# Optimization experiments

Hardware: AMD Instinct MI355X
Metric: run time of the kernel (lower is better)

## Reference

```python
import jax, jax.numpy as jnp
import numpy as np

B, L, V, D, H, DK, NL, M = 4, 1024, 64, 256, 4, 64, 4, 20
FF = 4 * D
EPS = 1e-5


def _rel_table(seq_len, m):
    # abs(i-j), log-bucketed beyond m, clipped to [0, 2m] -> int indices [L, L]
    d = jnp.abs(jnp.arange(seq_len)[:, None] - jnp.arange(seq_len)[None, :]).astype(jnp.float32)
    d = jnp.where(d > m, m + jnp.log2(jnp.maximum(d - m, 1.0)), d)
    return jnp.clip(d, 0, 2 * m).astype(jnp.int32)


def _layer_norm(x, g, b):
    mu = jnp.mean(x, axis=-1, keepdims=True)
    var = jnp.mean(jnp.square(x - mu), axis=-1, keepdims=True)
    return (x - mu) * jax.lax.rsqrt(var + EPS) * g + b


def setup_inputs() -> dict:
    key = jax.random.key(0)
    ks = jax.random.split(key, 16)
    w = lambda i, shape: jax.random.normal(ks[i], shape, jnp.float32) * 0.05
    return {
        "x": jax.random.normal(ks[0], (B, L, V), jnp.float32),
        "emb": w(1, (V, D)),
        "Wq": w(2, (NL, D, H * DK)), "bq": jnp.zeros((NL, H * DK), jnp.float32),
        "Wk": w(3, (NL, D, H * DK)), "bk": jnp.zeros((NL, H * DK), jnp.float32),
        "Wv": w(4, (NL, D, H * DK)), "bv": jnp.zeros((NL, H * DK), jnp.float32),
        "Wo": w(5, (NL, H * DK, D)), "bo": jnp.zeros((NL, D), jnp.float32),
        "rel_k": 1.0 + w(6, (NL, 2 * M + 1, H)),  # multiplicative bias ~1
        "rel_b": w(7, (NL, 2 * M + 1, H)),
        "ln1_g": jnp.ones((NL, D), jnp.float32), "ln1_b": jnp.zeros((NL, D), jnp.float32),
        "W1": w(8, (NL, D, FF)), "b1": jnp.zeros((NL, FF), jnp.float32),
        "W2": w(9, (NL, FF, D)), "b2": jnp.zeros((NL, D), jnp.float32),
        "ln2_g": jnp.ones((NL, D), jnp.float32), "ln2_b": jnp.zeros((NL, D), jnp.float32),
    }


def reference(x, emb, Wq, bq, Wk, bk, Wv, bv, Wo, bo, rel_k, rel_b,
              ln1_g, ln1_b, W1, b1, W2, b2, ln2_g, ln2_b):
    h = x @ emb  # [B, L, D]  (dropout inactive: eval mode)
    table = _rel_table(L, M)  # [L, L] int32
    inv_sqrt_dk = jnp.float32(1.0 / np.sqrt(DK))
    attns = []
    for l in range(NL):
        q = (h @ Wq[l] + bq[l]).reshape(B, L, H, DK)
        k = (h @ Wk[l] + bk[l]).reshape(B, L, H, DK)
        v = (h @ Wv[l] + bv[l]).reshape(B, L, H, DK)
        scores = jnp.einsum('blhk,bmhk->bhlm', q, k) * inv_sqrt_dk
        # per-head relative-position bias (table symmetric, so axis order of L,L is immaterial)
        bias_k = jnp.transpose(rel_k[l][table], (2, 1, 0))  # [H, L, L]
        bias_b = jnp.transpose(rel_b[l][table], (2, 1, 0))  # [H, L, L]
        scores = scores * bias_k[None] + bias_b[None]
        attn = jax.nn.softmax(scores, axis=-1)  # attn dropout inactive (eval)
        attns.append(attn)
        out = jnp.einsum('bhlm,bmhk->blhk', attn, v).reshape(B, L, H * DK) @ Wo[l] + bo[l]
        # FeedForwardNetwork (note: source has NO residual connections)
        y = _layer_norm(out, ln1_g[l], ln1_b[l])
        y = jax.nn.gelu(y @ W1[l] + b1[l], approximate=False) @ W2[l] + b2[l]
        h = _layer_norm(y, ln2_g[l], ln2_b[l])
    avg_attn = jnp.mean(jnp.stack(attns, axis=0), axis=0)  # [B, H, L, L]
    return h.mean(axis=1), avg_attn
```

## Files before the change

kernel.cpp:

```cpp
#include <hip/hip_runtime.h>
#include <hip/hip_bf16.h>
#include <math.h>

#define Bn 4
#define Ln 1024
#define Vn 64
#define Dn 256
#define Hn 4
#define DKn 64
#define NLn 4
#define Mn 20
#define FFn 1024
#define NTOK (Bn * Ln)
#define QKVW 768
#define LOG2E 1.4426950408889634f
#define PELEMS (Bn * Hn * Ln * Ln)

typedef __attribute__((ext_vector_type(8))) short bf16x8;
typedef __attribute__((ext_vector_type(4))) float f32x4;

__device__ __forceinline__ ushort f2b(float f) {
    uint u = __float_as_uint(f);
    u += 0x7fff + ((u >> 16) & 1);
    return (ushort)(u >> 16);
}
__device__ __forceinline__ float b2f(ushort u) {
    return __uint_as_float(((uint)u) << 16);
}

__global__ __launch_bounds__(256) void embed_k(const float* __restrict__ X,
                                               const float* __restrict__ E,
                                               ushort* __restrict__ Hb) {
    __shared__ float xs[Vn];
    int n = blockIdx.x, d = threadIdx.x;
    if (threadIdx.x < Vn) xs[threadIdx.x] = X[n * Vn + threadIdx.x];
    __syncthreads();
    float s = 0.f;
#pragma unroll
    for (int v = 0; v < Vn; ++v) s += xs[v] * E[v * Dn + d];
    Hb[(size_t)n * Dn + d] = f2b(s);
}

__global__ __launch_bounds__(256) void relbias_k(const float* __restrict__ rk,
                                                 const float* __restrict__ rb,
                                                 float* __restrict__ bkT,
                                                 float* __restrict__ bbT) {
    int tid = blockIdx.x * 256 + threadIdx.x;
    int dist = tid & 1023;
    int hh = (tid >> 10) & 3;
    int l = tid >> 12;
    float dd = (float)dist;
    if (dist > Mn) dd = (float)Mn + log2f((float)(dist - Mn));
    if (dd > 2.0f * Mn) dd = 2.0f * Mn;
    int idx = (int)dd;
    bkT[tid] = rk[(l * (2 * Mn + 1) + idx) * Hn + hh] * 0.125f * LOG2E;
    bbT[tid] = rb[(l * (2 * Mn + 1) + idx) * Hn + hh] * LOG2E;
}

__global__ __launch_bounds__(256) void prep_bias(const float* __restrict__ bq,
                                                 const float* __restrict__ bk,
                                                 const float* __restrict__ bv,
                                                 float* __restrict__ bqkv) {
    int idx = blockIdx.x * 256 + threadIdx.x;
    int l = idx / QKVW, r = idx - l * QKVW;
    float v;
    if (r < 256)      v = bq[l * 256 + r];
    else if (r < 512) v = bk[l * 256 + r - 256];
    else              v = bv[l * 256 + r - 512];
    bqkv[idx] = v;
}

__global__ __launch_bounds__(256) void transpose_cvt(
    const float* __restrict__ src, ushort* __restrict__ dst,
    int R, int C, int srcLS, int dstLS) {
    __shared__ float s[32][33];
    src += (size_t)blockIdx.z * srcLS;
    dst += (size_t)blockIdx.z * dstLS;
    int r0 = blockIdx.y * 32, c0 = blockIdx.x * 32;
    int tx = threadIdx.x & 31, ty = threadIdx.x >> 5;
#pragma unroll
    for (int ii = 0; ii < 4; ++ii)
        s[ty + 8 * ii][tx] = src[(size_t)(r0 + ty + 8 * ii) * C + c0 + tx];
    __syncthreads();
#pragma unroll
    for (int ii = 0; ii < 4; ++ii)
        dst[(size_t)(c0 + ty + 8 * ii) * R + r0 + tx] = f2b(s[tx][ty + 8 * ii]);
}

__global__ __launch_bounds__(256) void transpose_v(const ushort* __restrict__ qkv,
                                                   ushort* __restrict__ Vt) {
    __shared__ ushort s[32][65];
    int j0 = blockIdx.x * 32;
    int bh = blockIdx.y;
    int b = bh >> 2, hh = bh & 3;
    int t = threadIdx.x;
#pragma unroll
    for (int ii = 0; ii < 8; ++ii) {
        int e = t + 256 * ii;
        int jr = e >> 6, dc = e & 63;
        s[jr][dc] = qkv[(size_t)(b * Ln + j0 + jr) * QKVW + 2 * Dn + hh * DKn + dc];
    }
    __syncthreads();
#pragma unroll
    for (int ii = 0; ii < 8; ++ii) {
        int e = t + 256 * ii;
        int dr = e >> 5, jc = e & 31;
        Vt[(size_t)(bh * DKn + dr) * Ln + j0 + jc] = s[jc][dr];
    }
}

#define GST 40
#define GEMM_FRAG_MFMA                                                        \
    bf16x8 a0 = *(const bf16x8*)&As[(wm * 32 + l15) * GST + lg * 8];          \
    bf16x8 a1 = *(const bf16x8*)&As[(wm * 32 + 16 + l15) * GST + lg * 8];     \
    bf16x8 b0 = *(const bf16x8*)&Bs[(wn * 32 + l15) * GST + lg * 8];          \
    bf16x8 b1 = *(const bf16x8*)&Bs[(wn * 32 + 16 + l15) * GST + lg * 8];     \
    acc[0][0] = __builtin_amdgcn_mfma_f32_16x16x32_bf16(a0, b0, acc[0][0], 0, 0, 0); \
    acc[0][1] = __builtin_amdgcn_mfma_f32_16x16x32_bf16(a0, b1, acc[0][1], 0, 0, 0); \
    acc[1][0] = __builtin_amdgcn_mfma_f32_16x16x32_bf16(a1, b0, acc[1][0], 0, 0, 0); \
    acc[1][1] = __builtin_amdgcn_mfma_f32_16x16x32_bf16(a1, b1, acc[1][1], 0, 0, 0);

template <int LNA>
__global__ __launch_bounds__(256) void gemm_mfma(
    const ushort* __restrict__ A, const ushort* __restrict__ Bt,
    const float* __restrict__ bias, ushort* __restrict__ C,
    int M, int N, int K, int act,
    const float* __restrict__ lng, const float* __restrict__ lnb) {
    __shared__ __align__(16) ushort As[64 * GST];
    __shared__ __align__(16) ushort Bs[64 * GST];
    __shared__ float gl[256];
    __shared__ float bl[256];
    int t = threadIdx.x;
    int lane = t & 63, w = t >> 6;
    int wm = w >> 1, wn = w & 1;
    int l15 = lane & 15, lg = lane >> 4;
    int mBase = blockIdx.y * 64, nBase = blockIdx.x * 64;
    int lrow = t >> 2, lkc = (t & 3) * 8;
    const ushort* Ap = A + (size_t)(mBase + lrow) * K + lkc;
    const ushort* Bp = Bt + (size_t)(nBase + lrow) * K + lkc;
    f32x4 acc[2][2] = {};

    if constexpr (LNA) {
        uint4 areg[8];
        float s = 0.f;
#pragma unroll
        for (int kc = 0; kc < 8; ++kc) {
            areg[kc] = *(const uint4*)(Ap + kc * 32);
            const ushort* e = (const ushort*)&areg[kc];
#pragma unroll
            for (int q = 0; q < 8; ++q) s += b2f(e[q]);
        }
        s += __shfl_xor(s, 1, 64);
        s += __shfl_xor(s, 2, 64);
        float mu = s * (1.0f / 256.0f);
        float vv = 0.f;
#pragma unroll
        for (int kc = 0; kc < 8; ++kc) {
            const ushort* e = (const ushort*)&areg[kc];
#pragma unroll
            for (int q = 0; q < 8; ++q) {
                float d = b2f(e[q]) - mu;
                vv += d * d;
            }
        }
        vv += __shfl_xor(vv, 1, 64);
        vv += __shfl_xor(vv, 2, 64);
        float rs = rsqrtf(vv * (1.0f / 256.0f) + 1e-5f);
        gl[t] = lng[t];
        bl[t] = lnb[t];
        __syncthreads();
#pragma unroll
        for (int kc = 0; kc < 8; ++kc) {
            uint4 bv = *(const uint4*)(Bp + kc * 32);
            __syncthreads();
            {
                const ushort* e = (const ushort*)&areg[kc];
                ushort outv[8];
#pragma unroll
                for (int q = 0; q < 8; ++q) {
                    int col = kc * 32 + lkc + q;
                    outv[q] = f2b((b2f(e[q]) - mu) * rs * gl[col] + bl[col]);
                }
                *(uint4*)&As[lrow * GST + lkc] = *(const uint4*)outv;
            }
            *(uint4*)&Bs[lrow * GST + lkc] = bv;
            __syncthreads();
            GEMM_FRAG_MFMA
        }
    } else {
        for (int k0 = 0; k0 < K; k0 += 32) {
            uint4 av = *(const uint4*)(Ap + k0);
            uint4 bv = *(const uint4*)(Bp + k0);
            __syncthreads();
            *(uint4*)&As[lrow * GST + lkc] = av;
            *(uint4*)&Bs[lrow * GST + lkc] = bv;
            __syncthreads();
            GEMM_FRAG_MFMA
        }
    }
#pragma unroll
    for (int ni = 0; ni < 2; ++ni) {
        int col = nBase + wn * 32 + ni * 16 + l15;
        float bc = bias[col];
#pragma unroll
        for (int mi = 0; mi < 2; ++mi) {
            int rb = mBase + wm * 32 + mi * 16 + lg * 4;
#pragma unroll
            for (int j = 0; j < 4; ++j) {
                float v = acc[mi][ni][j] + bc;
                if (act) v = v * 0.5f * (1.0f + erff(v * 0.7071067811865475f));
                C[(size_t)(rb + j) * N + col] = f2b(v);
            }
        }
    }
}

#define PWST 40
#define NW 8
template <int MODE>
__global__ __launch_bounds__(512) void attn_fused(
    const ushort* __restrict__ qkv, const ushort* __restrict__ Vt,
    const float* __restrict__ bkTab, const float* __restrict__ bbTab,
    ushort* __restrict__ ctx, float* __restrict__ avg,
    ushort* __restrict__ Pout, int first) {
    __shared__ float bk_l[Ln];
    __shared__ float bb_l[Ln];
    __shared__ __align__(16) char uni[NW][4096];
    __shared__ float mm[NW][16];
    __shared__ float ll[NW][16];

    int t = threadIdx.x;
    int lane = t & 63, w = t >> 6;
    int wn = w & 3, wc = w >> 2;
    int l15 = lane & 15, lg = lane >> 4;

    ushort* pwh = (ushort*)&uni[w][0];
    ushort* pwl = (ushort*)&uni[w][1280];

    int bid = blockIdx.x;
    int xcd = bid & 7, sub = bid >> 3;
    int bh = xcd * 2 + (sub >> 6);
    int q = sub & 63;
    int b = bh >> 2, hh = bh & 3;
    int i0 = q * 16;

#pragma unroll
    for (int ii = 0; ii < 2; ++ii) {
        bk_l[t + 512 * ii] = bkTab[hh * Ln + t + 512 * ii];
        bb_l[t + 512 * ii] = bbTab[hh * Ln + t + 512 * ii];
    }
    __syncthreads();

    bf16x8 qa0, qa1;
    {
        const ushort* qp = qkv + (size_t)(b * Ln + i0 + l15) * QKVW + hh * DKn;
        qa0 = *(const bf16x8*)(qp + lg * 8);
        qa1 = *(const bf16x8*)(qp + 32 + lg * 8);
    }

    const ushort* kbase = qkv + (size_t)(b * Ln) * QKVW + Dn + hh * DKn;

    f32x4 sv[8];
    float m[4] = {-1e30f, -1e30f, -1e30f, -1e30f};
#pragma unroll
    for (int cl = 0; cl < 8; ++cl) {
        int c = wc * 8 + cl;
        const ushort* kp = kbase + (size_t)(c * 64 + wn * 16 + l15) * QKVW;
        bf16x8 k0 = *(const bf16x8*)(kp + lg * 8);
        bf16x8 k1 = *(const bf16x8*)(kp + 32 + lg * 8);
        f32x4 acc = {};
        acc = __builtin_amdgcn_mfma_f32_16x16x32_bf16(qa0, k0, acc, 0, 0, 0);
        acc = __builtin_amdgcn_mfma_f32_16x16x32_bf16(qa1, k1, acc, 0, 0, 0);
        int j = c * 64 + wn * 16 + l15;
#pragma unroll
        for (int r = 0; r < 4; ++r) {
            int i = i0 + lg * 4 + r;
            int dist = (i > j) ? (i - j) : (j - i);
            float s = acc[r] * bk_l[dist] + bb_l[dist];
            sv[cl][r] = s;
            m[r] = fmaxf(m[r], s);
        }
    }
#pragma unroll
    for (int mask = 1; mask < 16; mask <<= 1)
#pragma unroll
        for (int r = 0; r < 4; ++r) m[r] = fmaxf(m[r], __shfl_xor(m[r], mask, 64));
    if (l15 == 0)
#pragma unroll
        for (int r = 0; r < 4; ++r) mm[w][lg * 4 + r] = m[r];
    __syncthreads();
#pragma unroll
    for (int r = 0; r < 4; ++r) {
        int row = lg * 4 + r;
        float m0 = fmaxf(fmaxf(mm[0][row], mm[1][row]), fmaxf(mm[2][row], mm[3][row]));
        float m1 = fmaxf(fmaxf(mm[4][row], mm[5][row]), fmaxf(mm[6][row], mm[7][row]));
        m[r] = fmaxf(m0, m1);
    }
    float lsum[4] = {0.f, 0.f, 0.f, 0.f};
#pragma unroll
    for (int cl = 0; cl < 8; ++cl)
#pragma unroll
        for (int r = 0; r < 4; ++r) {
            float p = exp2f(sv[cl][r] - m[r]);
            sv[cl][r] = p;
            lsum[r] += p;
        }
#pragma unroll
    for (int mask = 1; mask < 16; mask <<= 1)
#pragma unroll
        for (int r = 0; r < 4; ++r) lsum[r] += __shfl_xor(lsum[r], mask, 64);
    if (l15 == 0)
#pragma unroll
        for (int r = 0; r < 4; ++r) ll[w][lg * 4 + r] = lsum[r];
    __syncthreads();
    float invl[4];
#pragma unroll
    for (int r = 0; r < 4; ++r) {
        int row = lg * 4 + r;
        invl[r] = 1.0f / (ll[0][row] + ll[1][row] + ll[2][row] + ll[3][row] +
                          ll[4][row] + ll[5][row] + ll[6][row] + ll[7][row]);
    }

    const ushort* vbase = Vt + (size_t)bh * DKn * Ln;
    float* avgrow = avg + ((size_t)bh * Ln + i0) * Ln;
    ushort* prow = Pout + ((size_t)bh * Ln + i0) * Ln;
    int iw = lane >> 2, jq = lane & 3;
    f32x4 acco[4] = {};
#pragma unroll
    for (int p = 0; p < 4; ++p) {
        const int c0 = wc * 8 + 2 * p, c1 = c0 + 1;
        float aold[2][4];
        if (MODE == 0 && !first) {
#pragma unroll
            for (int cc = 0; cc < 2; ++cc)
#pragma unroll
                for (int r = 0; r < 4; ++r)
                    aold[cc][r] = avgrow[(size_t)(lg * 4 + r) * Ln +
                                         (c0 + cc) * 64 + wn * 16 + l15];
        }
#pragma unroll
        for (int cc = 0; cc < 2; ++cc)
#pragma unroll
            for (int r = 0; r < 4; ++r) {
                float pv = sv[2 * p + cc][r] * invl[r];
                sv[2 * p + cc][r] = pv;
                ushort ph = f2b(pv);
                int off = (lg * 4 + r) * PWST + cc * 16 + l15;
                pwh[off] = ph;
                pwl[off] = f2b(pv - b2f(ph));
            }
        int kcol = (lg < 2 ? c0 : c1) * 64 + wn * 16 + (lg & 1) * 8;
        bf16x8 va0 = *(const bf16x8*)(vbase + (size_t)(0 * 16 + l15) * Ln + kcol);
        bf16x8 va1 = *(const bf16x8*)(vbase + (size_t)(1 * 16 + l15) * Ln + kcol);
        bf16x8 va2 = *(const bf16x8*)(vbase + (size_t)(2 * 16 + l15) * Ln + kcol);
        bf16x8 va3 = *(const bf16x8*)(vbase + (size_t)(3 * 16 + l15) * Ln + kcol);
        bf16x8 pbh = *(const bf16x8*)&pwh[l15 * PWST + lg * 8];
        bf16x8 pbl = *(const bf16x8*)&pwl[l15 * PWST + lg * 8];
        acco[0] = __builtin_amdgcn_mfma_f32_16x16x32_bf16(va0, pbh, acco[0], 0, 0, 0);
        acco[1] = __builtin_amdgcn_mfma_f32_16x16x32_bf16(va1, pbh, acco[1], 0, 0, 0);
        acco[2] = __builtin_amdgcn_mfma_f32_16x16x32_bf16(va2, pbh, acco[2], 0, 0, 0);
        acco[3] = __builtin_amdgcn_mfma_f32_16x16x32_bf16(va3, pbh, acco[3], 0, 0, 0);
        acco[0] = __builtin_amdgcn_mfma_f32_16x16x32_bf16(va0, pbl, acco[0], 0, 0, 0);
        acco[1] = __builtin_amdgcn_mfma_f32_16x16x32_bf16(va1, pbl, acco[1], 0, 0, 0);
        acco[2] = __builtin_amdgcn_mfma_f32_16x16x32_bf16(va2, pbl, acco[2], 0, 0, 0);
        acco[3] = __builtin_amdgcn_mfma_f32_16x16x32_bf16(va3, pbl, acco[3], 0, 0, 0);
        if (MODE == 0) {
#pragma unroll
            for (int cc = 0; cc < 2; ++cc)
#pragma unroll
                for (int r = 0; r < 4; ++r) {
                    float v = 0.25f * sv[2 * p + cc][r];
                    if (!first) v += aold[cc][r];
                    avgrow[(size_t)(lg * 4 + r) * Ln + (c0 + cc) * 64 + wn * 16 + l15] = v;
                }
        } else {
            ushort4 ph0 = *(const ushort4*)&pwh[iw * PWST + 0 * 16 + jq * 4];
            ushort4 ph1 = *(const ushort4*)&pwh[iw * PWST + 1 * 16 + jq * 4];
            *(ushort4*)&prow[(size_t)iw * Ln + c0 * 64 + wn * 16 + jq * 4] = ph0;
            *(ushort4*)&prow[(size_t)iw * Ln + c1 * 64 + wn * 16 + jq * 4] = ph1;
        }
    }

    {
        float* op = (float*)&uni[w][0];
#pragma unroll
        for (int dg = 0; dg < 4; ++dg)
#pragma unroll
            for (int r = 0; r < 4; ++r)
                op[(dg * 16 + lg * 4 + r) * 16 + l15] = acco[dg][r];
    }
    __syncthreads();
#pragma unroll
    for (int k = 0; k < 2; ++k) {
        int idx = t + 512 * k;
        float v = 0.f;
#pragma unroll
        for (int wv = 0; wv < NW; ++wv) v += ((const float*)&uni[wv][0])[idx];
        int dd = idx >> 4, ii = idx & 15;
        ctx[(size_t)(b * Ln + i0 + ii) * Dn + hh * DKn + dd] = f2b(v);
    }
}

__global__ __launch_bounds__(256) void avg_sum_k(const ushort* __restrict__ P,
                                                 float* __restrict__ avg) {
    size_t e = ((size_t)blockIdx.x * 256 + threadIdx.x) * 8;
    uint4 a = *(const uint4*)&P[e];
    uint4 b4 = *(const uint4*)&P[(size_t)PELEMS + e];
    uint4 c4 = *(const uint4*)&P[(size_t)2 * PELEMS + e];
    uint4 d4 = *(const uint4*)&P[(size_t)3 * PELEMS + e];
    const ushort* ap = (const ushort*)&a;
    const ushort* bp = (const ushort*)&b4;
    const ushort* cp = (const ushort*)&c4;
    const ushort* dp = (const ushort*)&d4;
    float4 o0, o1;
    float* o0p = (float*)&o0;
    float* o1p = (float*)&o1;
#pragma unroll
    for (int k = 0; k < 4; ++k)
        o0p[k] = 0.25f * (b2f(ap[k]) + b2f(bp[k]) + b2f(cp[k]) + b2f(dp[k]));
#pragma unroll
    for (int k = 0; k < 4; ++k)
        o1p[k] = 0.25f * (b2f(ap[4 + k]) + b2f(bp[4 + k]) + b2f(cp[4 + k]) + b2f(dp[4 + k]));
    *(float4*)&avg[e] = o0;
    *(float4*)&avg[e + 4] = o1;
}

__global__ __launch_bounds__(256) void layernorm_k(const ushort* __restrict__ X,
                                                   const float* __restrict__ g,
                                                   const float* __restrict__ bta,
                                                   ushort* __restrict__ Y) {
    int w = threadIdx.x >> 6, lane = threadIdx.x & 63;
    int row = blockIdx.x * 4 + w;
    const ushort* xr = X + (size_t)row * Dn;
    float x[4];
#pragma unroll
    for (int ii = 0; ii < 4; ++ii) x[ii] = b2f(xr[lane + 64 * ii]);
    float s = x[0] + x[1] + x[2] + x[3];
#pragma unroll
    for (int m = 1; m < 64; m <<= 1) s += __shfl_xor(s, m, 64);
    float mu = s * (1.0f / 256.0f);
    float vs = 0.f;
#pragma unroll
    for (int ii = 0; ii < 4; ++ii) {
        float d = x[ii] - mu;
        vs += d * d;
    }
#pragma unroll
    for (int m = 1; m < 64; m <<= 1) vs += __shfl_xor(vs, m, 64);
    float rs = rsqrtf(vs * (1.0f / 256.0f) + 1e-5f);
#pragma unroll
    for (int ii = 0; ii < 4; ++ii) {
        int d = lane + 64 * ii;
        Y[(size_t)row * Dn + d] = f2b((x[ii] - mu) * rs * g[d] + bta[d]);
    }
}

__global__ __launch_bounds__(256) void mean_part_k(const ushort* __restrict__ Hb,
                                                   float* __restrict__ part) {
    int blk = blockIdx.x;
    int b = blk >> 4, g = blk & 15;
    int d = threadIdx.x;
    float s = 0.f;
#pragma unroll
    for (int r = 0; r < 64; ++r)
        s += b2f(Hb[(size_t)(b * Ln + g * 64 + r) * Dn + d]);
    part[(size_t)blk * Dn + d] = s;
}
__global__ __launch_bounds__(256) void mean_final_k(const float* __restrict__ part,
                                                    float* __restrict__ out) {
    int b = blockIdx.x, d = threadIdx.x;
    float s = 0.f;
#pragma unroll
    for (int g = 0; g < 16; ++g) s += part[(size_t)(b * 16 + g) * Dn + d];
    out[b * Dn + d] = s * (1.0f / (float)Ln);
}

extern "C" void kernel_launch(void* const* d_in, const int* in_sizes, int n_in,
                              void* d_out, int out_size, void* d_ws, size_t ws_size,
                              hipStream_t stream) {
    const float* x    = (const float*)d_in[0];
    const float* emb  = (const float*)d_in[1];
    const float* Wq   = (const float*)d_in[2];
    const float* bq   = (const float*)d_in[3];
    const float* Wk   = (const float*)d_in[4];
    const float* bk   = (const float*)d_in[5];
    const float* Wv   = (const float*)d_in[6];
    const float* bv   = (const float*)d_in[7];
    const float* Wo   = (const float*)d_in[8];
    const float* bo   = (const float*)d_in[9];
    const float* rk   = (const float*)d_in[10];
    const float* rb   = (const float*)d_in[11];
    const float* ln1g = (const float*)d_in[12];
    const float* ln1b = (const float*)d_in[13];
    const float* W1   = (const float*)d_in[14];
    const float* b1   = (const float*)d_in[15];
    const float* W2   = (const float*)d_in[16];
    const float* b2   = (const float*)d_in[17];
    const float* ln2g = (const float*)d_in[18];
    const float* ln2b = (const float*)d_in[19];

    float* out = (float*)d_out;
    float* avg = out + Bn * Dn;

    char* ws = (char*)d_ws;
    const size_t MB = 1024 * 1024;
    ushort* hb   = (ushort*)(ws);
    ushort* qkvb = (ushort*)(ws + 2 * MB);
    ushort* ctxb = (ushort*)(ws + 8 * MB);
    ushort* t1   = (ushort*)(ws + 10 * MB);
    ushort* ffb  = (ushort*)(ws + 12 * MB);
    ushort* qkvT = (ushort*)(ws + 20 * MB);
    ushort* WoT  = (ushort*)(ws + 22 * MB);
    ushort* W1T  = (ushort*)(ws + 23 * MB);
    ushort* W2T  = (ushort*)(ws + 25 * MB);
    float*  bqkv = (float*)(ws + 27 * MB);
    float*  bkT  = (float*)(ws + 27 * MB + 65536);
    float*  bbT  = (float*)(ws + 27 * MB + 131072);
    ushort* Vt   = (ushort*)(ws + 30 * MB);
    float*  mpart= (float*)(ws + 33 * MB);
    ushort* Pbuf = (ushort*)(ws + 36 * MB);

    const size_t need = 36 * MB + (size_t)4 * PELEMS * sizeof(ushort);
    const bool fancy = (ws_size >= need);

    embed_k<<<NTOK, 256, 0, stream>>>(x, emb, hb);
    relbias_k<<<64, 256, 0, stream>>>(rk, rb, bkT, bbT);
    prep_bias<<<12, 256, 0, stream>>>(bq, bk, bv, bqkv);

    dim3 t88(8, 8, NLn);
    transpose_cvt<<<t88, 256, 0, stream>>>(Wq, qkvT + 0,      256, 256, 65536, 196608);
    transpose_cvt<<<t88, 256, 0, stream>>>(Wk, qkvT + 65536,  256, 256, 65536, 196608);
    transpose_cvt<<<t88, 256, 0, stream>>>(Wv, qkvT + 131072, 256, 256, 65536, 196608);
    transpose_cvt<<<t88, 256, 0, stream>>>(Wo, WoT,           256, 256, 65536, 65536);
    transpose_cvt<<<dim3(32, 8, NLn), 256, 0, stream>>>(W1, W1T, 256, 1024, 262144, 262144);
    transpose_cvt<<<dim3(8, 32, NLn), 256, 0, stream>>>(W2, W2T, 1024, 256, 262144, 262144);

    for (int l = 0; l < NLn; ++l) {
        if (l == 0) {
            gemm_mfma<0><<<dim3(12, 64), 256, 0, stream>>>(
                hb, qkvT + (size_t)l * 196608, bqkv + l * QKVW, qkvb,
                NTOK, QKVW, Dn, 0, nullptr, nullptr);
        } else {
            gemm_mfma<1><<<dim3(12, 64), 256, 0, stream>>>(
                hb, qkvT + (size_t)l * 196608, bqkv + l * QKVW, qkvb,
                NTOK, QKVW, Dn, 0, ln2g + (l - 1) * 256, ln2b + (l - 1) * 256);
        }
        transpose_v<<<dim3(32, 16), 256, 0, stream>>>(qkvb, Vt);
        if (fancy) {
            attn_fused<1><<<1024, 512, 0, stream>>>(
                qkvb, Vt, bkT + l * Hn * Ln, bbT + l * Hn * Ln, ctxb, avg,
                Pbuf + (size_t)l * PELEMS, (l == 0) ? 1 : 0);
        } else {
            attn_fused<0><<<1024, 512, 0, stream>>>(
                qkvb, Vt, bkT + l * Hn * Ln, bbT + l * Hn * Ln, ctxb, avg,
                (ushort*)Pbuf, (l == 0) ? 1 : 0);
        }
        gemm_mfma<0><<<dim3(4, 64), 256, 0, stream>>>(
            ctxb, WoT + (size_t)l * 65536, bo + l * 256, t1,
            NTOK, Dn, Dn, 0, nullptr, nullptr);
        gemm_mfma<1><<<dim3(16, 64), 256, 0, stream>>>(
            t1, W1T + (size_t)l * 262144, b1 + l * FFn, ffb,
            NTOK, FFn, Dn, 1, ln1g + l * 256, ln1b + l * 256);
        gemm_mfma<0><<<dim3(4, 64), 256, 0, stream>>>(
            ffb, W2T + (size_t)l * 262144, b2 + l * 256, hb,
            NTOK, Dn, FFn, 0, nullptr, nullptr);
    }
    layernorm_k<<<NTOK / 4, 256, 0, stream>>>(
        hb, ln2g + 3 * 256, ln2b + 3 * 256, hb);
    if (fancy) {
        avg_sum_k<<<PELEMS / (256 * 8), 256, 0, stream>>>(Pbuf, avg);
    }
    mean_part_k<<<64, 256, 0, stream>>>(hb, mpart);
    mean_final_k<<<Bn, 256, 0, stream>>>(mpart, out);
}
```

Measured before the change: 416.1 us.

## Fuse V transpose into QKV GEMM and attention-average into last layer

The QKV GEMM epilogue now writes V directly in transposed layout for the V column blocks, so the separate transpose_v kernel is gone. The last layer's attention kernel reads the three stored bf16 probability maps, adds its own, and writes the fp32 average itself. This removes the avg_sum_k pass and the fourth P buffer. The attention context reduction across warps now goes through two-stage shared-memory accumulation into four slots instead of eight, which adds extra barriers. The QKV GEMM skips its normal C store for V columns, which is fine only as long as attention reads V solely from Vt.

```diff
diff --git a/kernel.cpp b/kernel.cpp
--- a/kernel.cpp
+++ b/kernel.cpp
@@ -87,28 +87,6 @@
         dst[(size_t)(c0 + ty + 8 * ii) * R + r0 + tx] = f2b(s[tx][ty + 8 * ii]);
 }
 
-__global__ __launch_bounds__(256) void transpose_v(const ushort* __restrict__ qkv,
-                                                   ushort* __restrict__ Vt) {
-    __shared__ ushort s[32][65];
-    int j0 = blockIdx.x * 32;
-    int bh = blockIdx.y;
-    int b = bh >> 2, hh = bh & 3;
-    int t = threadIdx.x;
-#pragma unroll
-    for (int ii = 0; ii < 8; ++ii) {
-        int e = t + 256 * ii;
-        int jr = e >> 6, dc = e & 63;
-        s[jr][dc] = qkv[(size_t)(b * Ln + j0 + jr) * QKVW + 2 * Dn + hh * DKn + dc];
-    }
-    __syncthreads();
-#pragma unroll
-    for (int ii = 0; ii < 8; ++ii) {
-        int e = t + 256 * ii;
-        int dr = e >> 5, jc = e & 31;
-        Vt[(size_t)(bh * DKn + dr) * Ln + j0 + jc] = s[jc][dr];
-    }
-}
-
 #define GST 40
 #define GEMM_FRAG_MFMA                                                        \
     bf16x8 a0 = *(const bf16x8*)&As[(wm * 32 + l15) * GST + lg * 8];          \
@@ -125,7 +103,8 @@
     const ushort* __restrict__ A, const ushort* __restrict__ Bt,
     const float* __restrict__ bias, ushort* __restrict__ C,
     int M, int N, int K, int act,
-    const float* __restrict__ lng, const float* __restrict__ lnb) {
+    const float* __restrict__ lng, const float* __restrict__ lnb,
+    ushort* __restrict__ Vt_out) {
     __shared__ __align__(16) ushort As[64 * GST];
     __shared__ __align__(16) ushort Bs[64 * GST];
     __shared__ float gl[256];
@@ -198,6 +177,25 @@
             GEMM_FRAG_MFMA
         }
     }
+    if (Vt_out != nullptr && nBase >= 512) {
+#pragma unroll
+        for (int ni = 0; ni < 2; ++ni) {
+            int col = nBase + wn * 32 + ni * 16 + l15;
+            float bc = bias[col];
+            int d = col - 512;
+#pragma unroll
+            for (int mi = 0; mi < 2; ++mi) {
+                int rb = mBase + wm * 32 + mi * 16 + lg * 4;
+                int bb_ = rb >> 10, i_ = rb & 1023;
+                size_t vb = ((size_t)(bb_ * 4 + (d >> 6)) * 64 + (d & 63)) * Ln + i_;
+                ushort o4[4];
+#pragma unroll
+                for (int j = 0; j < 4; ++j) o4[j] = f2b(acc[mi][ni][j] + bc);
+                *(ushort4*)&Vt_out[vb] = *(const ushort4*)o4;
+            }
+        }
+        return;
+    }
 #pragma unroll
     for (int ni = 0; ni < 2; ++ni) {
         int col = nBase + wn * 32 + ni * 16 + l15;
@@ -225,7 +223,7 @@
     ushort* __restrict__ Pout, int first) {
     __shared__ float bk_l[Ln];
     __shared__ float bb_l[Ln];
-    __shared__ __align__(16) char uni[NW][4096];
+    __shared__ __align__(16) char uni[20480];
     __shared__ float mm[NW][16];
     __shared__ float ll[NW][16];
 
@@ -234,8 +232,8 @@
     int wn = w & 3, wc = w >> 2;
     int l15 = lane & 15, lg = lane >> 4;
 
-    ushort* pwh = (ushort*)&uni[w][0];
-    ushort* pwl = (ushort*)&uni[w][1280];
+    ushort* pwh = (ushort*)&uni[w * 2560];
+    ushort* pwl = (ushort*)&uni[w * 2560 + 1280];
 
     int bid = blockIdx.x;
     int xcd = bid & 7, sub = bid >> 3;
@@ -373,56 +371,66 @@
                     if (!first) v += aold[cc][r];
                     avgrow[(size_t)(lg * 4 + r) * Ln + (c0 + cc) * 64 + wn * 16 + l15] = v;
                 }
-        } else {
+        } else if (MODE == 1) {
             ushort4 ph0 = *(const ushort4*)&pwh[iw * PWST + 0 * 16 + jq * 4];
             ushort4 ph1 = *(const ushort4*)&pwh[iw * PWST + 1 * 16 + jq * 4];
             *(ushort4*)&prow[(size_t)iw * Ln + c0 * 64 + wn * 16 + jq * 4] = ph0;
             *(ushort4*)&prow[(size_t)iw * Ln + c1 * 64 + wn * 16 + jq * 4] = ph1;
-        }
-    }
-
+        } else {
+#pragma unroll
+            for (int cc = 0; cc < 2; ++cc) {
+                int c = c0 + cc;
+                size_t base = ((size_t)(bh * Ln) + i0 + iw) * Ln +
+                              c * 64 + wn * 16 + jq * 4;
+                ushort4 p0 = *(const ushort4*)&Pout[base];
+                ushort4 p1 = *(const ushort4*)&Pout[(size_t)PELEMS + base];
+                ushort4 p2 = *(const ushort4*)&Pout[(size_t)2 * PELEMS + base];
+                ushort4 p3 = *(const ushort4*)&pwh[iw * PWST + cc * 16 + jq * 4];
+                const ushort* q0 = (const ushort*)&p0;
+                const ushort* q1 = (const ushort*)&p1;
+                const ushort* q2 = (const ushort*)&p2;
+                const ushort* q3 = (const ushort*)&p3;
+                float4 o;
+                float* op_ = (float*)&o;
+#pragma unroll
+                for (int k = 0; k < 4; ++k)
+                    op_[k] = 0.25f * (b2f(q0[k]) + b2f(q1[k]) + b2f(q2[k]) + b2f(q3[k]));
+                *(float4*)&avg[base] = o;
+            }
+        }
+    }
+
+    __syncthreads();
     {
-        float* op = (float*)&uni[w][0];
-#pragma unroll
-        for (int dg = 0; dg < 4; ++dg)
-#pragma unroll
-            for (int r = 0; r < 4; ++r)
-                op[(dg * 16 + lg * 4 + r) * 16 + l15] = acco[dg][r];
+        float* op = (float*)&uni[wn * 4096];
+        if (wc == 1) {
+#pragma unroll
+            for (int dg = 0; dg < 4; ++dg)
+#pragma unroll
+                for (int r = 0; r < 4; ++r)
+                    op[(dg * 16 + lg * 4 + r) * 16 + l15] = acco[dg][r];
+        }
+    }
+    __syncthreads();
+    {
+        float* op = (float*)&uni[wn * 4096];
+        if (wc == 0) {
+#pragma unroll
+            for (int dg = 0; dg < 4; ++dg)
+#pragma unroll
+                for (int r = 0; r < 4; ++r)
+                    op[(dg * 16 + lg * 4 + r) * 16 + l15] += acco[dg][r];
+        }
     }
     __syncthreads();
 #pragma unroll
     for (int k = 0; k < 2; ++k) {
         int idx = t + 512 * k;
-        float v = 0.f;
-#pragma unroll
-        for (int wv = 0; wv < NW; ++wv) v += ((const float*)&uni[wv][0])[idx];
+        float v = ((const float*)&uni[0])[idx] + ((const float*)&uni[4096])[idx] +
+                  ((const float*)&uni[8192])[idx] + ((const float*)&uni[12288])[idx];
         int dd = idx >> 4, ii = idx & 15;
         ctx[(size_t)(b * Ln + i0 + ii) * Dn + hh * DKn + dd] = f2b(v);
     }
-}
-
-__global__ __launch_bounds__(256) void avg_sum_k(const ushort* __restrict__ P,
-                                                 float* __restrict__ avg) {
-    size_t e = ((size_t)blockIdx.x * 256 + threadIdx.x) * 8;
-    uint4 a = *(const uint4*)&P[e];
-    uint4 b4 = *(const uint4*)&P[(size_t)PELEMS + e];
-    uint4 c4 = *(const uint4*)&P[(size_t)2 * PELEMS + e];
-    uint4 d4 = *(const uint4*)&P[(size_t)3 * PELEMS + e];
-    const ushort* ap = (const ushort*)&a;
-    const ushort* bp = (const ushort*)&b4;
-    const ushort* cp = (const ushort*)&c4;
-    const ushort* dp = (const ushort*)&d4;
-    float4 o0, o1;
-    float* o0p = (float*)&o0;
-    float* o1p = (float*)&o1;
-#pragma unroll
-    for (int k = 0; k < 4; ++k)
-        o0p[k] = 0.25f * (b2f(ap[k]) + b2f(bp[k]) + b2f(cp[k]) + b2f(dp[k]));
-#pragma unroll
-    for (int k = 0; k < 4; ++k)
-        o1p[k] = 0.25f * (b2f(ap[4 + k]) + b2f(bp[4 + k]) + b2f(cp[4 + k]) + b2f(dp[4 + k]));
-    *(float4*)&avg[e] = o0;
-    *(float4*)&avg[e + 4] = o1;
 }
 
 __global__ __launch_bounds__(256) void layernorm_k(const ushort* __restrict__ X,
@@ -520,7 +528,7 @@
     float*  mpart= (float*)(ws + 33 * MB);
     ushort* Pbuf = (ushort*)(ws + 36 * MB);
 
-    const size_t need = 36 * MB + (size_t)4 * PELEMS * sizeof(ushort);
+    const size_t need = 36 * MB + (size_t)3 * PELEMS * sizeof(ushort);
     const bool fancy = (ws_size >= need);
 
     embed_k<<<NTOK, 256, 0, stream>>>(x, emb, hb);
@@ -539,17 +547,22 @@
         if (l == 0) {
             gemm_mfma<0><<<dim3(12, 64), 256, 0, stream>>>(
                 hb, qkvT + (size_t)l * 196608, bqkv + l * QKVW, qkvb,
-                NTOK, QKVW, Dn, 0, nullptr, nullptr);
+                NTOK, QKVW, Dn, 0, nullptr, nullptr, Vt);
         } else {
             gemm_mfma<1><<<dim3(12, 64), 256, 0, stream>>>(
                 hb, qkvT + (size_t)l * 196608, bqkv + l * QKVW, qkvb,
-                NTOK, QKVW, Dn, 0, ln2g + (l - 1) * 256, ln2b + (l - 1) * 256);
-        }
-        transpose_v<<<dim3(32, 16), 256, 0, stream>>>(qkvb, Vt);
+                NTOK, QKVW, Dn, 0, ln2g + (l - 1) * 256, ln2b + (l - 1) * 256, Vt);
+        }
         if (fancy) {
-            attn_fused<1><<<1024, 512, 0, stream>>>(
-                qkvb, Vt, bkT + l * Hn * Ln, bbT + l * Hn * Ln, ctxb, avg,
-                Pbuf + (size_t)l * PELEMS, (l == 0) ? 1 : 0);
+            if (l < 3) {
+                attn_fused<1><<<1024, 512, 0, stream>>>(
+                    qkvb, Vt, bkT + l * Hn * Ln, bbT + l * Hn * Ln, ctxb, avg,
+                    Pbuf + (size_t)l * PELEMS, 0);
+            } else {
+                attn_fused<2><<<1024, 512, 0, stream>>>(
+                    qkvb, Vt, bkT + l * Hn * Ln, bbT + l * Hn * Ln, ctxb, avg,
+                    Pbuf, 0);
+            }
         } else {
             attn_fused<0><<<1024, 512, 0, stream>>>(
                 qkvb, Vt, bkT + l * Hn * Ln, bbT + l * Hn * Ln, ctxb, avg,
@@ -557,19 +570,16 @@
         }
         gemm_mfma<0><<<dim3(4, 64), 256, 0, stream>>>(
             ctxb, WoT + (size_t)l * 65536, bo + l * 256, t1,
-            NTOK, Dn, Dn, 0, nullptr, nullptr);
+            NTOK, Dn, Dn, 0, nullptr, nullptr, nullptr);
         gemm_mfma<1><<<dim3(16, 64), 256, 0, stream>>>(
             t1, W1T + (size_t)l * 262144, b1 + l * FFn, ffb,
-            NTOK, FFn, Dn, 1, ln1g + l * 256, ln1b + l * 256);
+            NTOK, FFn, Dn, 1, ln1g + l * 256, ln1b + l * 256, nullptr);
         gemm_mfma<0><<<dim3(4, 64), 256, 0, stream>>>(
             ffb, W2T + (size_t)l * 262144, b2 + l * 256, hb,
-            NTOK, Dn, FFn, 0, nullptr, nullptr);
+            NTOK, Dn, FFn, 0, nullptr, nullptr, nullptr);
     }
     layernorm_k<<<NTOK / 4, 256, 0, stream>>>(
         hb, ln2g + 3 * 256, ln2b + 3 * 256, hb);
-    if (fancy) {
-        avg_sum_k<<<PELEMS / (256 * 8), 256, 0, stream>>>(Pbuf, avg);
-    }
     mean_part_k<<<64, 256, 0, stream>>>(hb, mpart);
     mean_final_k<<<Bn, 256, 0, stream>>>(mpart, out);
 }
```

After: 391.8 us. 5.8% less time.
